# Kernel tuning notes

Hardware: AMD Instinct MI355X
Metric: run time of the kernel (lower is better)

## Reference

```python
import jax, jax.numpy as jnp
import numpy as np

N_NODES = 50000
D_IN = 128
D_OUT = 64
N_ETYPES = 3
E_PER_ETYPE = 500000
P_ETYPE = 0.5  # self.p[etype] init value for every etype


def setup_inputs() -> dict:
    key = jax.random.key(0)
    k1, k2, k3, k4 = jax.random.split(key, 4)
    feat = jax.random.normal(k1, (N_NODES, D_IN), dtype=jnp.float32)
    W = jax.random.normal(k2, (D_IN, D_OUT), dtype=jnp.float32) * 0.05
    b = jax.random.normal(k3, (D_OUT,), dtype=jnp.float32) * 0.05
    # edge_index[e] = (src, dst) for etype e
    edge_index = jax.random.randint(k4, (N_ETYPES, 2, E_PER_ETYPE), 0, N_NODES, dtype=jnp.int64)
    return {"feat": feat, "W": W, "b": b, "edge_index": edge_index}


def reference(feat, W, b, edge_index):
    N = feat.shape[0]

    def agg_one_etype(ei):
        src, dst = ei[0], ei[1]
        # scatter-mean of src features onto dst nodes (dgl copy_u + mean)
        msg_sum = jax.ops.segment_sum(feat[src], dst, num_segments=N)          # [N, D]
        cnt = jax.ops.segment_sum(jnp.ones(src.shape, feat.dtype), dst, num_segments=N)
        hr = msg_sum / jnp.maximum(cnt, 1.0)[:, None]  # zero-in-degree nodes -> 0
        return jnp.tanh(hr)  # per-etype activation

    hr_all = jax.vmap(agg_one_etype)(edge_index)        # [n_etypes, N, D]
    h_homo = jnp.sum(hr_all * P_ETYPE, axis=0) + feat   # weighted sum + residual
    h_homo = jnp.tanh(h_homo)
    return h_homo @ W + b                               # final linear
```

## Files before the change

### kernel.cpp

```cpp
#include <hip/hip_runtime.h>
#include <hip/hip_bf16.h>

#define N_NODES 50000
#define D_IN 128
#define D_OUT 64
#define N_ETYPES 3
#define E_PER_ETYPE 500000
#define N_EDGES (N_ETYPES * E_PER_ETYPE)
#define CAP1 16
#define CAP2 30
#define DMAX (CAP1 + CAP2)
#define ZROW N_NODES
#define NB_FEAT ((N_NODES * D_IN / 4) / 256)
#define NB_W ((D_IN * D_OUT) / 256)
#define NZINT4 ((N_ETYPES * N_NODES + 16) / 4)
#define NB_ZCNT ((NZINT4 + 255) / 256)
#define CHUNK_EDGES 2048
#define N_CHUNKS ((N_EDGES + CHUNK_EDGES - 1) / CHUNK_EDGES)
#define NSLICE 8
#define SLICE_N 6250
#define QCAP 196608
#define NBLK_PER_SLICE 64

typedef __attribute__((ext_vector_type(8))) short short8;
typedef __attribute__((ext_vector_type(4))) float f32x4;

static __device__ __forceinline__ unsigned short f2bf(float f) {
    unsigned int x = __float_as_uint(f);
    unsigned int lsb = (x >> 16) & 1u;
    x += 0x7fffu + lsb;
    return (unsigned short)(x >> 16);
}

static __device__ __forceinline__ float fast_tanh(float x) {
    float e = __expf(2.0f * x);
    return 1.0f - 2.0f * __builtin_amdgcn_rcpf(e + 1.0f);
}

static __device__ __forceinline__ short8 as_s8(uint4 u) {
    union { uint4 u; short8 s; } cv; cv.u = u; return cv.s;
}

static __device__ __forceinline__ void accum8(float* ax, uint4 p) {
    ax[0] += __uint_as_float(p.x << 16);
    ax[1] += __uint_as_float(p.x & 0xffff0000u);
    ax[2] += __uint_as_float(p.y << 16);
    ax[3] += __uint_as_float(p.y & 0xffff0000u);
    ax[4] += __uint_as_float(p.z << 16);
    ax[5] += __uint_as_float(p.z & 0xffff0000u);
    ax[6] += __uint_as_float(p.w << 16);
    ax[7] += __uint_as_float(p.w & 0xffff0000u);
}

static __device__ __forceinline__ float2 rs_reduce(const float* ax, int sub) {
    bool hi = (sub & 1);
    float k0_ = hi ? ax[4] : ax[0], s0_ = hi ? ax[0] : ax[4];
    float k1_ = hi ? ax[5] : ax[1], s1_ = hi ? ax[1] : ax[5];
    float k2_ = hi ? ax[6] : ax[2], s2_ = hi ? ax[2] : ax[6];
    float k3_ = hi ? ax[7] : ax[3], s3_ = hi ? ax[3] : ax[7];
    float h0 = k0_ + __shfl_xor(s0_, 16);
    float h1 = k1_ + __shfl_xor(s1_, 16);
    float h2 = k2_ + __shfl_xor(s2_, 16);
    float h3 = k3_ + __shfl_xor(s3_, 16);
    bool hi2 = (sub & 2);
    float ka = hi2 ? h2 : h0, sa = hi2 ? h0 : h2;
    float kb = hi2 ? h3 : h1, sb = hi2 ? h1 : h3;
    float2 v;
    v.x = ka + __shfl_xor(sa, 32);
    v.y = kb + __shfl_xor(sb, 32);
    return v;
}

__global__ __launch_bounds__(256) void convert_kernel(
    const float* __restrict__ feat,
    unsigned short* __restrict__ featbf,
    const float* __restrict__ W,
    unsigned short* __restrict__ wtbf,
    int* __restrict__ cnt)
{
    int b = blockIdx.x;
    if (b < NB_FEAT) {
        int i = b * 256 + threadIdx.x;
        const float4* f4 = (const float4*)feat;
        float4 v = f4[i];
        ushort4 o;
        o.x = f2bf(v.x); o.y = f2bf(v.y); o.z = f2bf(v.z); o.w = f2bf(v.w);
        ((ushort4*)featbf)[i] = o;
    } else if (b < NB_FEAT + NB_W) {
        int i = (b - NB_FEAT) * 256 + threadIdx.x;
        int n = i >> 7;
        int k = i & 127;
        wtbf[i] = f2bf(W[k * D_OUT + n]);
    } else if (b == NB_FEAT + NB_W) {
        if (threadIdx.x < 64)
            ((unsigned int*)(featbf + (size_t)N_NODES * D_IN))[threadIdx.x] = 0;
    } else {
        int i = (b - NB_FEAT - NB_W - 1) * 256 + threadIdx.x;
        if (i < NZINT4) {
            int4 z; z.x = 0; z.y = 0; z.z = 0; z.w = 0;
            ((int4*)cnt)[i] = z;
        }
    }
}

__global__ __launch_bounds__(256) void fill_kernel(
    const int* __restrict__ edge_index,
    unsigned short* __restrict__ bucket1,
    unsigned short* __restrict__ spill,
    int* __restrict__ cnt)
{
    int slice = blockIdx.x & 7;
    int chunk = blockIdx.x >> 3;
    int e0 = chunk * CHUNK_EDGES + threadIdx.x;
    #pragma unroll
    for (int k = 0; k < CHUNK_EDGES / 256; k++) {
        int e = e0 + k * 256;
        if (e < N_EDGES) {
            int t  = e / E_PER_ETYPE;
            int ei = e - t * E_PER_ETYPE;
            const int* base = edge_index + (long long)t * 2 * E_PER_ETYPE;
            int dst = __builtin_nontemporal_load(base + E_PER_ETYPE + ei);
            int s = (int)(((unsigned long long)(unsigned)dst * 687195ull) >> 32);
            if (s == slice) {
                int src = __builtin_nontemporal_load(base + ei);
                int cell = t * N_NODES + dst;
                int pos = atomicAdd(cnt + cell, 1);
                if (pos < CAP1)
                    bucket1[cell * CAP1 + pos] = (unsigned short)src;
                else if (pos < CAP1 + CAP2)
                    spill[cell * CAP2 + (pos - CAP1)] = (unsigned short)src;
            }
        }
    }
}

__global__ __launch_bounds__(256) void partition_kernel(
    const int* __restrict__ edge_index,
    unsigned int* __restrict__ queue,
    int* __restrict__ qcnt)
{
    __shared__ int lcnt[NSLICE];
    __shared__ int lbase[NSLICE];
    int tid = threadIdx.x;
    if (tid < NSLICE) lcnt[tid] = 0;
    __syncthreads();
    int e0 = blockIdx.x * CHUNK_EDGES + tid;
    unsigned int rec[CHUNK_EDGES / 256];
    int sl[CHUNK_EDGES / 256], pos[CHUNK_EDGES / 256];
    #pragma unroll
    for (int k = 0; k < CHUNK_EDGES / 256; k++) {
        int e = e0 + k * 256;
        sl[k] = -1;
        if (e < N_EDGES) {
            int t  = e / E_PER_ETYPE;
            int ei = e - t * E_PER_ETYPE;
            const int* base = edge_index + (long long)t * 2 * E_PER_ETYPE;
            int src = __builtin_nontemporal_load(base + ei);
            int dst = __builtin_nontemporal_load(base + E_PER_ETYPE + ei);
            int s = (int)(((unsigned long long)(unsigned)dst * 687195ull) >> 32);
            int ldst = dst - s * SLICE_N;
            rec[k] = (unsigned)src | ((unsigned)ldst << 16) | ((unsigned)t << 29);
            sl[k]  = s;
            pos[k] = atomicAdd(&lcnt[s], 1);
        }
    }
    __syncthreads();
    if (tid < NSLICE) lbase[tid] = atomicAdd(&qcnt[tid], lcnt[tid]);
    __syncthreads();
    #pragma unroll
    for (int k = 0; k < CHUNK_EDGES / 256; k++) {
        if (sl[k] >= 0) {
            int p = lbase[sl[k]] + pos[k];
            if (p < QCAP)
                queue[sl[k] * QCAP + p] = rec[k];
        }
    }
}

__global__ __launch_bounds__(256) void binfill_kernel(
    const unsigned int* __restrict__ queue,
    const int* __restrict__ qcnt,
    unsigned short* __restrict__ bucket1,
    unsigned short* __restrict__ spill,
    int* __restrict__ cnt)
{
    int slice = blockIdx.x & 7;
    int blk   = blockIdx.x >> 3;
    int total = qcnt[slice];
    const unsigned int* q = queue + slice * QCAP;
    int sbase = slice * SLICE_N;
    for (int i = blk * 256 + threadIdx.x; i < total; i += NBLK_PER_SLICE * 256) {
        unsigned int r = __builtin_nontemporal_load(q + i);
        int src  = r & 0xFFFF;
        int ldst = (r >> 16) & 0x1FFF;
        int t    = r >> 29;
        int cell = t * N_NODES + sbase + ldst;
        int p = atomicAdd(cnt + cell, 1);
        if (p < CAP1)
            bucket1[cell * CAP1 + p] = (unsigned short)src;
        else if (p < DMAX)
            spill[cell * CAP2 + (p - CAP1)] = (unsigned short)src;
    }
}

__global__ __launch_bounds__(512) void gather_linear_kernel(
    const float* __restrict__ feat,
    const unsigned short* __restrict__ featbf,
    const unsigned short* __restrict__ wtbf,
    const float* __restrict__ bg,
    const unsigned short* __restrict__ bucket1,
    const unsigned short* __restrict__ spill,
    const int* __restrict__ cnt,
    float* __restrict__ out)
{
    __shared__ unsigned short hsb[16 * 128];

    int tid = threadIdx.x;
    int wave = tid >> 6;
    int lane = tid & 63;
    int sub  = lane >> 4;
    int sl   = lane & 15;
    int n0 = blockIdx.x * 16 + wave * 2;
    int n1 = n0 + 1;

    int degA[N_ETYPES], degB[N_ETYPES], idxA[N_ETYPES], idxB[N_ETYPES];
    #pragma unroll
    for (int t = 0; t < N_ETYPES; t++) {
        int cell = t * N_NODES + n0;
        unsigned long long dgp = __builtin_nontemporal_load(
            (const unsigned long long*)(cnt + cell));
        int dgx = (int)(dgp & 0xffffffffull);
        int dgy = (int)(dgp >> 32);
        int la = 0, lb = 0;
        if (lane < CAP1) {
            la = __builtin_nontemporal_load(bucket1 + cell * CAP1 + lane);
            lb = __builtin_nontemporal_load(bucket1 + (cell + 1) * CAP1 + lane);
        } else if (lane < DMAX) {
            if (dgx > CAP1) la = __builtin_nontemporal_load(spill + cell * CAP2 + (lane - CAP1));
            if (dgy > CAP1) lb = __builtin_nontemporal_load(spill + (cell + 1) * CAP2 + (lane - CAP1));
        }
        int ca = dgx < DMAX ? dgx : DMAX;
        int cb = dgy < DMAX ? dgy : DMAX;
        idxA[t] = (lane < ca) ? la : ZROW;
        idxB[t] = (lane < cb) ? lb : ZROW;
        degA[t] = dgx; degB[t] = dgy;
    }

    int k0 = ((sub & 1) << 2) | (sub & 2);
    int p2 = 4 * sl + (k0 >> 1);
    unsigned int rfA = ((const unsigned int*)featbf)[n0 * 64 + p2];
    unsigned int rfB = ((const unsigned int*)featbf)[n1 * 64 + p2];

    const uint4* fb4 = (const uint4*)featbf;
    float s0A = 0.0f, s1A = 0.0f, s0B = 0.0f, s1B = 0.0f;

    #pragma unroll
    for (int t = 0; t < N_ETYPES; t++) {
        int da = degA[t] < DMAX ? degA[t] : DMAX;
        int db = degB[t] < DMAX ? degB[t] : DMAX;
        int dm = da > db ? da : db;
        float axA[8], axB[8];
        #pragma unroll
        for (int k = 0; k < 8; k++) { axA[k] = 0.0f; axB[k] = 0.0f; }
        for (int j = 0; j < dm; j += 8) {
            int r0 = j + sub;
            int r1 = j + 4 + sub;
            int sa0 = __shfl(idxA[t], r0);
            int sa1 = __shfl(idxA[t], r1);
            int sb0 = __shfl(idxB[t], r0);
            int sb1 = __shfl(idxB[t], r1);
            uint4 pa0 = fb4[sa0 * 16 + sl];
            uint4 pa1 = fb4[sa1 * 16 + sl];
            uint4 pb0 = fb4[sb0 * 16 + sl];
            uint4 pb1 = fb4[sb1 * 16 + sl];
            accum8(axA, pa0); accum8(axA, pa1);
            accum8(axB, pb0); accum8(axB, pb1);
        }
        float2 vA = rs_reduce(axA, sub);
        float2 vB = rs_reduce(axB, sub);
        float invA = __builtin_amdgcn_rcpf((float)(degA[t] > 0 ? degA[t] : 1));
        float invB = __builtin_amdgcn_rcpf((float)(degB[t] > 0 ? degB[t] : 1));
        s0A += fast_tanh(vA.x * invA);
        s1A += fast_tanh(vA.y * invA);
        s0B += fast_tanh(vB.x * invB);
        s1B += fast_tanh(vB.y * invB);
    }

    float fAx = __uint_as_float(rfA << 16);
    float fAy = __uint_as_float(rfA & 0xffff0000u);
    float fBx = __uint_as_float(rfB << 16);
    float fBy = __uint_as_float(rfB & 0xffff0000u);
    float hxA = fast_tanh(fAx + 0.5f * s0A);
    float hyA = fast_tanh(fAy + 0.5f * s1A);
    float hxB = fast_tanh(fBx + 0.5f * s0B);
    float hyB = fast_tanh(fBy + 0.5f * s1B);
    unsigned int hpA = (unsigned int)f2bf(hxA) | ((unsigned int)f2bf(hyA) << 16);
    unsigned int hpB = (unsigned int)f2bf(hxB) | ((unsigned int)f2bf(hyB) << 16);
    int colb = 16 * sl + 2 * k0;
    int rA = wave * 2, rB = rA + 1;
    ((unsigned int*)hsb)[(rA * 256 + (colb ^ ((rA & 7) << 4))) >> 2] = hpA;
    ((unsigned int*)hsb)[(rB * 256 + (colb ^ ((rB & 7) << 4))) >> 2] = hpB;

    uint4 b0 = {0,0,0,0}, b1 = {0,0,0,0}, b2 = {0,0,0,0}, b3 = {0,0,0,0};
    float bias = 0.0f;
    if (wave < 4) {
        int nrow = wave * 16 + sl;
        const uint4* wt4 = (const uint4*)wtbf;
        b0 = wt4[nrow * 16 +  0 + sub];
        b1 = wt4[nrow * 16 +  4 + sub];
        b2 = wt4[nrow * 16 +  8 + sub];
        b3 = wt4[nrow * 16 + 12 + sub];
        bias = bg[nrow];
    }
    __syncthreads();

    if (wave < 4) {
        int row = sl;
        int rbase = row * 256;
        int rx = (row & 7) << 4;
        const uint4* h4 = (const uint4*)hsb;
        uint4 a0 = h4[(rbase + (( 0 + sub * 16) ^ rx)) >> 4];
        uint4 a1 = h4[(rbase + (( 64 + sub * 16) ^ rx)) >> 4];
        uint4 a2 = h4[(rbase + ((128 + sub * 16) ^ rx)) >> 4];
        uint4 a3 = h4[(rbase + ((192 + sub * 16) ^ rx)) >> 4];

        f32x4 c = {bias, bias, bias, bias};
        c = __builtin_amdgcn_mfma_f32_16x16x32_bf16(as_s8(a0), as_s8(b0), c, 0, 0, 0);
        c = __builtin_amdgcn_mfma_f32_16x16x32_bf16(as_s8(a1), as_s8(b1), c, 0, 0, 0);
        c = __builtin_amdgcn_mfma_f32_16x16x32_bf16(as_s8(a2), as_s8(b2), c, 0, 0, 0);
        c = __builtin_amdgcn_mfma_f32_16x16x32_bf16(as_s8(a3), as_s8(b3), c, 0, 0, 0);

        #pragma unroll
        for (int i = 0; i < 4; i++) {
            int orow = sub * 4 + i;
            out[(blockIdx.x * 16 + orow) * 64 + wave * 16 + sl] = c[i];
        }
    }
}

extern "C" void kernel_launch(void* const* d_in, const int* in_sizes, int n_in,
                              void* d_out, int out_size, void* d_ws, size_t ws_size,
                              hipStream_t stream) {
    const float* feat = (const float*)d_in[0];
    const float* W    = (const float*)d_in[1];
    const float* b    = (const float*)d_in[2];
    const int* edge_index = (const int*)d_in[3];
    float* out = (float*)d_out;

    size_t featbf_bytes  = (size_t)(N_NODES + 1) * D_IN * sizeof(unsigned short);
    size_t bucket1_bytes = (size_t)N_ETYPES * N_NODES * CAP1 * sizeof(unsigned short);
    size_t spill_bytes   = (size_t)N_ETYPES * N_NODES * CAP2 * sizeof(unsigned short);
    size_t cnt_bytes     = (size_t)(N_ETYPES * N_NODES + 16) * sizeof(int);
    size_t wtbf_bytes    = (size_t)D_IN * D_OUT * sizeof(unsigned short);
    size_t base_bytes    = featbf_bytes + bucket1_bytes + spill_bytes + cnt_bytes + wtbf_bytes;
    if (ws_size < base_bytes)
        return;

    unsigned short* featbf  = (unsigned short*)d_ws;
    unsigned short* bucket1 = (unsigned short*)((char*)d_ws + featbf_bytes);
    unsigned short* spill   = (unsigned short*)((char*)d_ws + featbf_bytes + bucket1_bytes);
    int* cnt = (int*)((char*)d_ws + featbf_bytes + bucket1_bytes + spill_bytes);
    unsigned short* wtbf = (unsigned short*)((char*)d_ws + featbf_bytes + bucket1_bytes
                                             + spill_bytes + cnt_bytes);

    convert_kernel<<<NB_FEAT + NB_W + 1 + NB_ZCNT, 256, 0, stream>>>(
        feat, featbf, W, wtbf, cnt);

    fill_kernel<<<N_CHUNKS * 8, 256, 0, stream>>>(edge_index, bucket1, spill, cnt);

    gather_linear_kernel<<<N_NODES / 16, 512, 0, stream>>>(
        feat, featbf, wtbf, b, bucket1, spill, cnt, out);
}
```

Measured before the change: 210.7 us.

## Replace global-atomic bucket fill with counting-sort histogram, offsets, and LDS placement

Replaces the global-atomic bucket fill with a three-pass counting sort. The passes are a per-(range, slice) histogram of destinations in shared memory, a prefix over ranges that yields per-cell offsets and counts, and a placement pass that uses shared-memory atomics to write sources into buckets. The aim is to remove contended global atomics on the count array. In exchange, dst indices are read twice and two extra launches are added, and per-range counts are stored as bytes, which could overflow if a cell gets more than 255 edges in a range. The new path runs only when the workspace is large enough, and the removed partition/binfill kernels were unused.

After: 237.6 us. +12.8%, slower.

```diff
diff --git a/kernel.cpp b/kernel.cpp
--- a/kernel.cpp
+++ b/kernel.cpp
@@ -19,11 +19,13 @@
 #define N_CHUNKS ((N_EDGES + CHUNK_EDGES - 1) / CHUNK_EDGES)
 #define NSLICE 8
 #define SLICE_N 6250
-#define QCAP 196608
-#define NBLK_PER_SLICE 64
+#define NRANGE 30
+#define EPR (E_PER_ETYPE / 10)
+#define CELLS_PER_SLICE (N_ETYPES * SLICE_N)
 
 typedef __attribute__((ext_vector_type(8))) short short8;
 typedef __attribute__((ext_vector_type(4))) float f32x4;
+typedef __attribute__((ext_vector_type(4))) int i32x4;
 
 static __device__ __forceinline__ unsigned short f2bf(float f) {
     unsigned int x = __float_as_uint(f);
@@ -103,6 +105,98 @@
     }
 }
 
+
+__global__ __launch_bounds__(512) void histo_kernel(
+    const int* __restrict__ edge_index,
+    unsigned char* __restrict__ partial)
+{
+    __shared__ int h[CELLS_PER_SLICE];
+    int tid = threadIdx.x;
+    int slice = blockIdx.x & 7;
+    int range = blockIdx.x >> 3;
+    int t  = range / 10;
+    int rb = range - t * 10;
+    const i32x4* d4p = (const i32x4*)(edge_index + (long long)t * 2 * E_PER_ETYPE
+                                      + E_PER_ETYPE + rb * EPR);
+    for (int i = tid; i < CELLS_PER_SLICE; i += 512) h[i] = 0;
+    __syncthreads();
+    int tsub = t * SLICE_N;
+    for (int i = tid; i < EPR / 4; i += 512) {
+        i32x4 d = __builtin_nontemporal_load(d4p + i);
+        #pragma unroll
+        for (int j = 0; j < 4; j++) {
+            int dst = d[j];
+            int s = (int)(((unsigned long long)(unsigned)dst * 687195ull) >> 32);
+            if (s == slice) atomicAdd(&h[tsub + dst - s * SLICE_N], 1);
+        }
+    }
+    __syncthreads();
+    unsigned char* p = partial + ((size_t)slice * NRANGE + range) * CELLS_PER_SLICE;
+    for (int i = tid; i < CELLS_PER_SLICE; i += 512)
+        p[i] = (unsigned char)h[i];
+}
+
+__global__ __launch_bounds__(512) void offsets_kernel(
+    unsigned char* __restrict__ partial,
+    int* __restrict__ cnt)
+{
+    int slice = blockIdx.x & 7;
+    int g = blockIdx.x >> 3;
+    int c = g * 512 + threadIdx.x;
+    if (c >= CELLS_PER_SLICE) return;
+    unsigned char* p = partial + (size_t)slice * NRANGE * CELLS_PER_SLICE + c;
+    int run = 0;
+    #pragma unroll
+    for (int b = 0; b < NRANGE; b++) {
+        int v = p[(size_t)b * CELLS_PER_SLICE];
+        p[(size_t)b * CELLS_PER_SLICE] = (unsigned char)run;
+        run += v;
+    }
+    int t = c / SLICE_N;
+    int ldst = c - t * SLICE_N;
+    cnt[t * N_NODES + slice * SLICE_N + ldst] = run;
+}
+
+__global__ __launch_bounds__(512) void place_kernel(
+    const int* __restrict__ edge_index,
+    const unsigned char* __restrict__ partial,
+    unsigned short* __restrict__ bucket1,
+    unsigned short* __restrict__ spill)
+{
+    __shared__ int cur[CELLS_PER_SLICE];
+    int tid = threadIdx.x;
+    int slice = blockIdx.x & 7;
+    int range = blockIdx.x >> 3;
+    int t  = range / 10;
+    int rb = range - t * 10;
+    const int* base = edge_index + (long long)t * 2 * E_PER_ETYPE;
+    int ei0 = rb * EPR;
+    const unsigned char* p = partial + ((size_t)slice * NRANGE + range) * CELLS_PER_SLICE;
+    for (int i = tid; i < CELLS_PER_SLICE; i += 512) cur[i] = p[i];
+    __syncthreads();
+    int tsub = t * SLICE_N;
+    int coff = t * N_NODES + slice * SLICE_N;
+    const i32x4* d4p = (const i32x4*)(base + E_PER_ETYPE + ei0);
+    for (int i = tid; i < EPR / 4; i += 512) {
+        i32x4 d = __builtin_nontemporal_load(d4p + i);
+        #pragma unroll
+        for (int j = 0; j < 4; j++) {
+            int dst = d[j];
+            int s = (int)(((unsigned long long)(unsigned)dst * 687195ull) >> 32);
+            if (s == slice) {
+                int ldst = dst - s * SLICE_N;
+                int src = __builtin_nontemporal_load(base + ei0 + i * 4 + j);
+                int pos = atomicAdd(&cur[tsub + ldst], 1);
+                int cell = coff + ldst;
+                if (pos < CAP1)
+                    bucket1[cell * CAP1 + pos] = (unsigned short)src;
+                else if (pos < DMAX)
+                    spill[cell * CAP2 + (pos - CAP1)] = (unsigned short)src;
+            }
+        }
+    }
+}
+
 __global__ __launch_bounds__(256) void fill_kernel(
     const int* __restrict__ edge_index,
     unsigned short* __restrict__ bucket1,
@@ -134,75 +228,6 @@
     }
 }
 
-__global__ __launch_bounds__(256) void partition_kernel(
-    const int* __restrict__ edge_index,
-    unsigned int* __restrict__ queue,
-    int* __restrict__ qcnt)
-{
-    __shared__ int lcnt[NSLICE];
-    __shared__ int lbase[NSLICE];
-    int tid = threadIdx.x;
-    if (tid < NSLICE) lcnt[tid] = 0;
-    __syncthreads();
-    int e0 = blockIdx.x * CHUNK_EDGES + tid;
-    unsigned int rec[CHUNK_EDGES / 256];
-    int sl[CHUNK_EDGES / 256], pos[CHUNK_EDGES / 256];
-    #pragma unroll
-    for (int k = 0; k < CHUNK_EDGES / 256; k++) {
-        int e = e0 + k * 256;
-        sl[k] = -1;
-        if (e < N_EDGES) {
-            int t  = e / E_PER_ETYPE;
-            int ei = e - t * E_PER_ETYPE;
-            const int* base = edge_index + (long long)t * 2 * E_PER_ETYPE;
-            int src = __builtin_nontemporal_load(base + ei);
-            int dst = __builtin_nontemporal_load(base + E_PER_ETYPE + ei);
-            int s = (int)(((unsigned long long)(unsigned)dst * 687195ull) >> 32);
-            int ldst = dst - s * SLICE_N;
-            rec[k] = (unsigned)src | ((unsigned)ldst << 16) | ((unsigned)t << 29);
-            sl[k]  = s;
-            pos[k] = atomicAdd(&lcnt[s], 1);
-        }
-    }
-    __syncthreads();
-    if (tid < NSLICE) lbase[tid] = atomicAdd(&qcnt[tid], lcnt[tid]);
-    __syncthreads();
-    #pragma unroll
-    for (int k = 0; k < CHUNK_EDGES / 256; k++) {
-        if (sl[k] >= 0) {
-            int p = lbase[sl[k]] + pos[k];
-            if (p < QCAP)
-                queue[sl[k] * QCAP + p] = rec[k];
-        }
-    }
-}
-
-__global__ __launch_bounds__(256) void binfill_kernel(
-    const unsigned int* __restrict__ queue,
-    const int* __restrict__ qcnt,
-    unsigned short* __restrict__ bucket1,
-    unsigned short* __restrict__ spill,
-    int* __restrict__ cnt)
-{
-    int slice = blockIdx.x & 7;
-    int blk   = blockIdx.x >> 3;
-    int total = qcnt[slice];
-    const unsigned int* q = queue + slice * QCAP;
-    int sbase = slice * SLICE_N;
-    for (int i = blk * 256 + threadIdx.x; i < total; i += NBLK_PER_SLICE * 256) {
-        unsigned int r = __builtin_nontemporal_load(q + i);
-        int src  = r & 0xFFFF;
-        int ldst = (r >> 16) & 0x1FFF;
-        int t    = r >> 29;
-        int cell = t * N_NODES + sbase + ldst;
-        int p = atomicAdd(cnt + cell, 1);
-        if (p < CAP1)
-            bucket1[cell * CAP1 + p] = (unsigned short)src;
-        else if (p < DMAX)
-            spill[cell * CAP2 + (p - CAP1)] = (unsigned short)src;
-    }
-}
-
 __global__ __launch_bounds__(512) void gather_linear_kernel(
     const float* __restrict__ feat,
     const unsigned short* __restrict__ featbf,
@@ -353,8 +378,10 @@
     size_t cnt_bytes     = (size_t)(N_ETYPES * N_NODES + 16) * sizeof(int);
     size_t wtbf_bytes    = (size_t)D_IN * D_OUT * sizeof(unsigned short);
     size_t base_bytes    = featbf_bytes + bucket1_bytes + spill_bytes + cnt_bytes + wtbf_bytes;
+    size_t partial_bytes = (size_t)NSLICE * NRANGE * CELLS_PER_SLICE;
     if (ws_size < base_bytes)
         return;
+    bool counting = (ws_size >= base_bytes + partial_bytes);
 
     unsigned short* featbf  = (unsigned short*)d_ws;
     unsigned short* bucket1 = (unsigned short*)((char*)d_ws + featbf_bytes);
@@ -362,11 +389,20 @@
     int* cnt = (int*)((char*)d_ws + featbf_bytes + bucket1_bytes + spill_bytes);
     unsigned short* wtbf = (unsigned short*)((char*)d_ws + featbf_bytes + bucket1_bytes
                                              + spill_bytes + cnt_bytes);
+    unsigned char* partial = (unsigned char*)d_ws + base_bytes;
 
     convert_kernel<<<NB_FEAT + NB_W + 1 + NB_ZCNT, 256, 0, stream>>>(
         feat, featbf, W, wtbf, cnt);
 
-    fill_kernel<<<N_CHUNKS * 8, 256, 0, stream>>>(edge_index, bucket1, spill, cnt);
+    if (counting) {
+        histo_kernel<<<NRANGE * NSLICE, 512, 0, stream>>>(edge_index, partial);
+        offsets_kernel<<<((CELLS_PER_SLICE + 511) / 512) * NSLICE, 512, 0, stream>>>(
+            partial, cnt);
+        place_kernel<<<NRANGE * NSLICE, 512, 0, stream>>>(
+            edge_index, partial, bucket1, spill);
+    } else {
+        fill_kernel<<<N_CHUNKS * 8, 256, 0, stream>>>(edge_index, bucket1, spill, cnt);
+    }
 
     gather_linear_kernel<<<N_NODES / 16, 512, 0, stream>>>(
         feat, featbf, wtbf, b, bucket1, spill, cnt, out);
```
